# Optimization experiments

Measured on AMD Instinct MI355X. Metric: run time of the kernel, lower is better.

Reference implementation:

```python
import jax, jax.numpy as jnp
import numpy as np

B, S, C, D, H, FF, DEPTH, T, N = 8, 1024, 2, 512, 8, 2048, 6, 64, 16
HD = D // H
EPS = 1e-5


def _ln(x, w, b):
    m = jnp.mean(x, axis=-1, keepdims=True)
    v = jnp.mean(jnp.square(x - m), axis=-1, keepdims=True)
    return (x - m) * jax.lax.rsqrt(v + EPS) * w + b


def setup_inputs() -> dict:
    key = jax.random.key(0)
    ks = jax.random.split(key, 24)
    w = lambda k, shape: (jax.random.normal(k, shape, jnp.float32) * 0.02)
    return {
        "src": jax.random.normal(ks[0], (B, S, D), jnp.float32),
        "ctx_emb": jax.random.normal(ks[1], (B, C, D), jnp.float32),
        "times": jax.random.randint(ks[2], (B, S), 0, T),
        "spaces": jax.random.randint(ks[3], (B, S), 0, N),
        "pad_mask": jnp.zeros((B, S + C), bool),
        "time_emb": w(ks[4], (T, D)),
        "space_emb": w(ks[5], (N, D)),
        "Wqkv": w(ks[6], (DEPTH, 3 * D, D)),
        "bqkv": jnp.zeros((DEPTH, 3 * D), jnp.float32),
        "Wo": w(ks[7], (DEPTH, D, D)),
        "bo": jnp.zeros((DEPTH, D), jnp.float32),
        "ln1_w": jnp.ones((DEPTH, D), jnp.float32),
        "ln1_b": jnp.zeros((DEPTH, D), jnp.float32),
        "W1": w(ks[8], (DEPTH, FF, D)),
        "b1": jnp.zeros((DEPTH, FF), jnp.float32),
        "W2": w(ks[9], (DEPTH, D, FF)),
        "b2": jnp.zeros((DEPTH, D), jnp.float32),
        "ln2_w": jnp.ones((DEPTH, D), jnp.float32),
        "ln2_b": jnp.zeros((DEPTH, D), jnp.float32),
    }


def _forward(src, ctx_emb, times, spaces, pad_mask, time_emb, space_emb,
             Wqkv, bqkv, Wo, bo, ln1_w, ln1_b, W1, b1, W2, b2, ln2_w, ln2_b):
    NEG = -jnp.inf
    # learned time/space positional embeddings, then append context tokens
    x = src + time_emb[times] + space_emb[spaces]          # [B,S,D]
    x = jnp.concatenate([x, ctx_emb], axis=1)              # [B,L,D], L=S+C
    # per-batch additive float mask: causal-in-time over src tokens,
    # ctx tokens attendable by everyone, ctx rows attend only to ctx.
    cond = times[:, :, None] >= times[:, None, :]          # [B,S,S]
    m = jnp.where(cond, 0.0, NEG)
    m = jnp.pad(m, ((0, 0), (0, C), (0, 0)), constant_values=NEG)  # ctx rows
    m = jnp.pad(m, ((0, 0), (0, 0), (0, C)), constant_values=0.0)  # ctx cols
    m = m + jnp.where(pad_mask[:, None, :], NEG, 0.0)      # key padding
    m = m[:, None]                                         # [B,1,L,L]

    scale = 1.0 / np.sqrt(HD)
    Bc, L, _ = x.shape
    for i in range(DEPTH):
        # --- self-attention (post-norm encoder layer) ---
        qkv = x @ Wqkv[i].T + bqkv[i]                      # [B,L,3D]
        q, k, v = jnp.split(qkv, 3, axis=-1)
        split = lambda t: t.reshape(Bc, L, H, HD).transpose(0, 2, 1, 3)
        q, k, v = split(q), split(k), split(v)             # [B,H,L,HD]
        scores = jnp.einsum('bhqd,bhkd->bhqk', q, k) * scale + m
        p = jax.nn.softmax(scores, axis=-1)
        a = jnp.einsum('bhqk,bhkd->bhqd', p, v)
        a = a.transpose(0, 2, 1, 3).reshape(Bc, L, D)
        a = a @ Wo[i].T + bo[i]
        x = _ln(x + a, ln1_w[i], ln1_b[i])
        # --- feed-forward ---
        h = jax.nn.gelu(x @ W1[i].T + b1[i], approximate=False)
        h = h @ W2[i].T + b2[i]
        x = _ln(x + h, ln2_w[i], ln2_b[i])
    return x[:, :S]                                        # drop ctx tokens


def reference(src, ctx_emb, times, spaces, pad_mask, time_emb, space_emb,
              Wqkv, bqkv, Wo, bo, ln1_w, ln1_b, W1, b1, W2, b2, ln2_w, ln2_b):
    return _forward(src, ctx_emb, times, spaces, pad_mask, time_emb, space_emb,
                    Wqkv, bqkv, Wo, bo, ln1_w, ln1_b, W1, b1, W2, b2, ln2_w, ln2_b)
```

## Files before the change

### kernel.cpp

```cpp
#include <hip/hip_runtime.h>
#include <hip/hip_bf16.h>

#define BB 8
#define SS 1024
#define CC 2
#define DD 512
#define NH 8
#define FF2 2048
#define NL 6
#define LL 1026
#define HD 64
#define MROWS 8208
#define MP 8320
#define KVPAD 1152

typedef __attribute__((ext_vector_type(8))) short bf16x8;
typedef __attribute__((ext_vector_type(4))) float f32x4;

typedef __attribute__((address_space(3))) void lds_void;
typedef __attribute__((address_space(1))) void g_void;

__device__ __forceinline__ void gll16(const void* g, void* l) {
  __builtin_amdgcn_global_load_lds((const g_void*)g, (lds_void*)l, 16, 0, 0);
}

__global__ __launch_bounds__(256) void cvt_bf16_k(const float* __restrict__ in,
                                                  __hip_bfloat16* __restrict__ out) {
  int i = (blockIdx.x * 256 + threadIdx.x) * 4;
  float4 v = *(const float4*)&in[i];
  out[i + 0] = __float2bfloat16(v.x);
  out[i + 1] = __float2bfloat16(v.y);
  out[i + 2] = __float2bfloat16(v.z);
  out[i + 3] = __float2bfloat16(v.w);
}

__global__ __launch_bounds__(256) void embed_k(const float* __restrict__ src,
    const float* __restrict__ ctx, const int* __restrict__ times,
    const int* __restrict__ spaces, const float* __restrict__ te,
    const float* __restrict__ se, float* __restrict__ x,
    __hip_bfloat16* __restrict__ xb) {
  int row = blockIdx.x;
  int b = row / LL, l = row % LL;
  int c = threadIdx.x * 2;
  float y0, y1;
  if (l < SS) {
    const float* sp = src + ((size_t)(b * SS + l)) * DD + c;
    int tt = times[b * SS + l], ssp = spaces[b * SS + l];
    y0 = sp[0] + te[tt * DD + c] + se[ssp * DD + c];
    y1 = sp[1] + te[tt * DD + c + 1] + se[ssp * DD + c + 1];
  } else {
    const float* cp = ctx + ((size_t)(b * CC + (l - SS))) * DD + c;
    y0 = cp[0]; y1 = cp[1];
  }
  size_t o = (size_t)row * DD + c;
  x[o] = y0; x[o + 1] = y1;
  xb[o] = __float2bfloat16(y0); xb[o + 1] = __float2bfloat16(y1);
}

template <int EPI>
__global__ __launch_bounds__(256) void gemm_bt(const __hip_bfloat16* __restrict__ A,
    const __hip_bfloat16* __restrict__ W, const float* __restrict__ bias,
    void* __restrict__ outp, int K, int N) {
  __shared__ __hip_bfloat16 As[128 * 64];
  __shared__ __hip_bfloat16 Bs[128 * 64];
  const int tid = threadIdx.x;
  const int lane = tid & 63, wv = tid >> 6;
  const int m0 = blockIdx.x * 128, n0 = blockIdx.y * 128;
  const int wr = wv >> 1, wc = wv & 1;
  const int r0 = lane & 15, kq = lane >> 4;
  f32x4 acc[4][4] = {};
  for (int k0 = 0; k0 < K; k0 += 64) {
    __syncthreads();
#pragma unroll
    for (int c = 0; c < 4; ++c) {
      int chb = c * 256 + wv * 64;
      int ch = chb + lane;
      int row = ch >> 3, cp = ch & 7;
      gll16(A + (size_t)(m0 + row) * K + k0 + cp * 8, (char*)As + chb * 16);
      gll16(W + (size_t)(n0 + row) * K + k0 + cp * 8, (char*)Bs + chb * 16);
    }
    __syncthreads();
#pragma unroll
    for (int kk = 0; kk < 64; kk += 32) {
      bf16x8 af[4], bfr[4];
#pragma unroll
      for (int m = 0; m < 4; ++m)
        af[m] = *(const bf16x8*)&As[(wr * 64 + m * 16 + r0) * 64 + kk + kq * 8];
#pragma unroll
      for (int n = 0; n < 4; ++n)
        bfr[n] = *(const bf16x8*)&Bs[(wc * 64 + n * 16 + r0) * 64 + kk + kq * 8];
#pragma unroll
      for (int m = 0; m < 4; ++m)
#pragma unroll
        for (int n = 0; n < 4; ++n)
          acc[m][n] = __builtin_amdgcn_mfma_f32_16x16x32_bf16(af[m], bfr[n], acc[m][n], 0, 0, 0);
    }
  }
#pragma unroll
  for (int m = 0; m < 4; ++m) {
    int grow_base = m0 + wr * 64 + m * 16 + kq * 4;
#pragma unroll
    for (int n = 0; n < 4; ++n) {
      int gcol = n0 + wc * 64 + n * 16 + r0;
      float bv = bias[gcol];
#pragma unroll
      for (int j = 0; j < 4; ++j) {
        int grow = grow_base + j;
        float v = acc[m][n][j] + bv;
        if (EPI == 2) v = 0.5f * v * (1.f + erff(v * 0.70710678f));
        if (EPI == 0)
          ((float*)outp)[(size_t)grow * N + gcol] = v;
        else
          ((__hip_bfloat16*)outp)[(size_t)grow * N + gcol] = __float2bfloat16(v);
      }
    }
  }
}

__global__ __launch_bounds__(256) void vtrans_k(const __hip_bfloat16* __restrict__ qkv,
                                                __hip_bfloat16* __restrict__ vt) {
  __shared__ __hip_bfloat16 tile[64][72];
  int bh = blockIdx.y;
  int b = bh >> 3, hh = bh & 7;
  int l0 = blockIdx.x * 64;
  int t = threadIdx.x;
  int lr = t >> 2, part = t & 3;
  int l = l0 + lr;
  if (l < LL) {
    const __hip_bfloat16* p = qkv + (size_t)(b * LL + l) * 1536 + 1024 + hh * 64 + part * 16;
    *(uint4*)&tile[lr][part * 16] = *(const uint4*)p;
    *(uint4*)&tile[lr][part * 16 + 8] = *(const uint4*)(p + 8);
  } else {
    uint4 z = make_uint4(0, 0, 0, 0);
    *(uint4*)&tile[lr][part * 16] = z;
    *(uint4*)&tile[lr][part * 16 + 8] = z;
  }
  __syncthreads();
  int d = t >> 2, kp = t & 3;
  __hip_bfloat16 vals[16];
#pragma unroll
  for (int i = 0; i < 16; ++i) vals[i] = tile[kp * 16 + i][d];
  __hip_bfloat16* o = vt + ((size_t)(bh * 64 + d)) * KVPAD + l0 + kp * 16;
  *(uint4*)o = *(uint4*)&vals[0];
  *(uint4*)(o + 8) = *(uint4*)&vals[8];
}

#define TK_CTX (-2000000000)
#define TQ_CTX (-1000000000)
#define TK_INV (2000000000)

__global__ __launch_bounds__(256) void attn_k(const __hip_bfloat16* __restrict__ qkv,
    const __hip_bfloat16* __restrict__ vt, const int* __restrict__ times,
    __hip_bfloat16* __restrict__ aout) {
  __shared__ __hip_bfloat16 Kl[128 * 64];
  __shared__ __hip_bfloat16 Vl[64 * 128];
  __shared__ __hip_bfloat16 Pl[4][16 * 128];
  const int tid = threadIdx.x, lane = tid & 63, wv = tid >> 6;
  const int r0 = lane & 15, kq = lane >> 4;
  int i = blockIdx.x;
  int xcd = i & 7, slot = i >> 3;
  int bhl = slot / 17;
  int qb = slot - bhl * 17;
  int bh = xcd * 8 + bhl;
  int b = bh >> 3, hh = bh & 7;
  char* plbase = (char*)&Pl[wv][0];

  const int qbase = qb * 64 + wv * 16;
  int qr = qbase + r0;
  if (qr > LL - 1) qr = LL - 1;
  const __hip_bfloat16* qp = qkv + (size_t)(b * LL + qr) * 1536 + hh * 64;
  bf16x8 qa0 = *(const bf16x8*)(qp + kq * 8);
  bf16x8 qa1 = *(const bf16x8*)(qp + 32 + kq * 8);
  int tq[4];
#pragma unroll
  for (int j = 0; j < 4; ++j) {
    int r = qbase + kq * 4 + j;
    tq[j] = (r < SS) ? times[b * SS + r] : TQ_CTX;
  }
  float m_run[4] = {-1e30f, -1e30f, -1e30f, -1e30f};
  float l_run[4] = {0.f, 0.f, 0.f, 0.f};
  f32x4 O[4] = {};
  const float scale = 0.125f;

  for (int kc = 0; kc < 9; ++kc) {
    __syncthreads();
#pragma unroll
    for (int c = 0; c < 4; ++c) {
      int chb = c * 256 + wv * 64;
      int ch = chb + lane;
      {
        int trow = ch >> 3, cp = ch & 7;
        int krow = kc * 128 + trow;
        if (krow > LL - 1) krow = LL - 1;
        int scp = cp ^ (trow & 7);
        gll16(qkv + (size_t)(b * LL + krow) * 1536 + 512 + hh * 64 + scp * 8,
              (char*)Kl + chb * 16);
      }
      {
        int d = ch >> 4, kp = ch & 15;
        int skp = kp ^ (d & 7);
        gll16(vt + ((size_t)(bh * 64 + d)) * KVPAD + kc * 128 + skp * 8,
              (char*)Vl + chb * 16);
      }
    }
    __syncthreads();
    f32x4 s[8] = {};
#pragma unroll
    for (int n = 0; n < 8; ++n) {
      int row = n * 16 + r0;
      bf16x8 kb0 = *(const bf16x8*)&Kl[row * 64 + ((kq ^ (row & 7)) * 8)];
      bf16x8 kb1 = *(const bf16x8*)&Kl[row * 64 + (((4 + kq) ^ (row & 7)) * 8)];
      s[n] = __builtin_amdgcn_mfma_f32_16x16x32_bf16(qa0, kb0, s[n], 0, 0, 0);
      s[n] = __builtin_amdgcn_mfma_f32_16x16x32_bf16(qa1, kb1, s[n], 0, 0, 0);
    }
    int tkn[8];
#pragma unroll
    for (int n = 0; n < 8; ++n) {
      int k = kc * 128 + 16 * n + r0;
      tkn[n] = (k < SS) ? times[b * SS + k] : ((k < LL) ? TK_CTX : TK_INV);
    }
    float mch[4] = {-1e30f, -1e30f, -1e30f, -1e30f};
#pragma unroll
    for (int n = 0; n < 8; ++n)
#pragma unroll
      for (int j = 0; j < 4; ++j) {
        float sv = (tq[j] >= tkn[n]) ? s[n][j] * scale : -1e30f;
        s[n][j] = sv;
        mch[j] = fmaxf(mch[j], sv);
      }
#pragma unroll
    for (int j = 0; j < 4; ++j) {
#pragma unroll
      for (int off = 1; off < 16; off <<= 1)
        mch[j] = fmaxf(mch[j], __shfl_xor(mch[j], off, 64));
    }
    float fac[4], psum[4];
#pragma unroll
    for (int j = 0; j < 4; ++j) {
      float mn = fmaxf(m_run[j], mch[j]);
      fac[j] = __expf(m_run[j] - mn);
      m_run[j] = mn;
      psum[j] = 0.f;
    }
#pragma unroll
    for (int n = 0; n < 8; ++n)
#pragma unroll
      for (int j = 0; j < 4; ++j) {
        float p = __expf(s[n][j] - m_run[j]);
        s[n][j] = p;
        psum[j] += p;
      }
#pragma unroll
    for (int j = 0; j < 4; ++j) {
#pragma unroll
      for (int off = 1; off < 16; off <<= 1)
        psum[j] += __shfl_xor(psum[j], off, 64);
      l_run[j] = l_run[j] * fac[j] + psum[j];
    }
#pragma unroll
    for (int n = 0; n < 4; ++n)
#pragma unroll
      for (int j = 0; j < 4; ++j) O[n][j] *= fac[j];
#pragma unroll
    for (int n = 0; n < 8; ++n)
#pragma unroll
      for (int j = 0; j < 4; ++j) {
        int q = kq * 4 + j;
        int byte = ((r0 + 16 * n) * 2) ^ ((q & 7) << 4);
        *(__hip_bfloat16*)(plbase + q * 256 + byte) = __float2bfloat16(s[n][j]);
      }
#pragma unroll
    for (int c = 0; c < 4; ++c) {
      int rbyte = (c * 64 + kq * 16) ^ ((r0 & 7) << 4);
      bf16x8 pa = *(const bf16x8*)(plbase + r0 * 256 + rbyte);
#pragma unroll
      for (int n = 0; n < 4; ++n) {
        int d = n * 16 + r0;
        int chv = (c * 4 + kq) ^ (r0 & 7);
        bf16x8 vb = *(const bf16x8*)&Vl[d * 128 + chv * 8];
        O[n] = __builtin_amdgcn_mfma_f32_16x16x32_bf16(pa, vb, O[n], 0, 0, 0);
      }
    }
  }
#pragma unroll
  for (int j = 0; j < 4; ++j) {
    int orow = qbase + kq * 4 + j;
    if (orow < LL) {
      float inv = 1.f / l_run[j];
#pragma unroll
      for (int n = 0; n < 4; ++n)
        aout[(size_t)(b * LL + orow) * DD + hh * 64 + n * 16 + r0] =
            __float2bfloat16(O[n][j] * inv);
    }
  }
}

__global__ __launch_bounds__(256) void ln_fuse_k(float* __restrict__ x,
    const float* __restrict__ tmp, const float* __restrict__ w,
    const float* __restrict__ bias, __hip_bfloat16* __restrict__ xb) {
  const int row = blockIdx.x;
  const int tid = threadIdx.x;
  size_t o = (size_t)row * DD + tid * 2;
  float2 v = *(const float2*)&x[o];
  float2 t = *(const float2*)&tmp[o];
  float a0 = v.x + t.x, a1 = v.y + t.y;
  float s = a0 + a1, ss = a0 * a0 + a1 * a1;
#pragma unroll
  for (int off = 1; off < 64; off <<= 1) {
    s += __shfl_xor(s, off, 64);
    ss += __shfl_xor(ss, off, 64);
  }
  __shared__ float red[8];
  const int wv = tid >> 6, lane = tid & 63;
  if (lane == 0) { red[wv] = s; red[4 + wv] = ss; }
  __syncthreads();
  s = red[0] + red[1] + red[2] + red[3];
  ss = red[4] + red[5] + red[6] + red[7];
  float mean = s * (1.f / 512.f);
  float var = ss * (1.f / 512.f) - mean * mean;
  if (var < 0.f) var = 0.f;
  float rs = rsqrtf(var + 1e-5f);
  float w0 = w[tid * 2], w1 = w[tid * 2 + 1];
  float b0 = bias[tid * 2], b1 = bias[tid * 2 + 1];
  float y0 = (a0 - mean) * rs * w0 + b0;
  float y1 = (a1 - mean) * rs * w1 + b1;
  x[o] = y0; x[o + 1] = y1;
  xb[o] = __float2bfloat16(y0); xb[o + 1] = __float2bfloat16(y1);
}

__global__ __launch_bounds__(256) void copy_out_k(const float* __restrict__ x,
                                                  float* __restrict__ out) {
  size_t i = ((size_t)blockIdx.x * 256 + threadIdx.x) * 4;
  int b = (int)(i >> 19);
  int rem = (int)(i & 524287);
  float4 v = *(const float4*)&x[(size_t)b * LL * DD + rem];
  *(float4*)&out[i] = v;
}

extern "C" void kernel_launch(void* const* d_in, const int* in_sizes, int n_in,
                              void* d_out, int out_size, void* d_ws, size_t ws_size,
                              hipStream_t stream) {
  (void)in_sizes; (void)n_in; (void)out_size; (void)ws_size;
  const float* src    = (const float*)d_in[0];
  const float* ctx    = (const float*)d_in[1];
  const int*   times  = (const int*)d_in[2];
  const int*   spaces = (const int*)d_in[3];
  const float* te     = (const float*)d_in[5];
  const float* se     = (const float*)d_in[6];
  const float* Wqkv   = (const float*)d_in[7];
  const float* bqkv   = (const float*)d_in[8];
  const float* Wo     = (const float*)d_in[9];
  const float* bo     = (const float*)d_in[10];
  const float* ln1w   = (const float*)d_in[11];
  const float* ln1b   = (const float*)d_in[12];
  const float* W1     = (const float*)d_in[13];
  const float* b1     = (const float*)d_in[14];
  const float* W2     = (const float*)d_in[15];
  const float* b2     = (const float*)d_in[16];
  const float* ln2w   = (const float*)d_in[17];
  const float* ln2b   = (const float*)d_in[18];

  char* ws = (char*)d_ws;
  size_t off = 0;
  auto alloc = [&](size_t bytes) {
    size_t o = off;
    off += (bytes + 255) & ~(size_t)255;
    return o;
  };
  float* x            = (float*)(ws + alloc((size_t)MP * DD * 4));
  __hip_bfloat16* xb  = (__hip_bfloat16*)(ws + alloc((size_t)MP * DD * 2));
  __hip_bfloat16* qkv = (__hip_bfloat16*)(ws + alloc((size_t)MP * 3 * DD * 2));
  __hip_bfloat16* abf = (__hip_bfloat16*)(ws + alloc((size_t)MP * DD * 2));
  __hip_bfloat16* hbf = (__hip_bfloat16*)(ws + alloc((size_t)MP * FF2 * 2));
  float* tmp          = (float*)(ws + alloc((size_t)MP * DD * 4));
  __hip_bfloat16* vt  = (__hip_bfloat16*)(ws + alloc((size_t)BB * NH * HD * KVPAD * 2));
  __hip_bfloat16* wqb = (__hip_bfloat16*)(ws + alloc((size_t)NL * 3 * DD * DD * 2));
  __hip_bfloat16* wob = (__hip_bfloat16*)(ws + alloc((size_t)NL * DD * DD * 2));
  __hip_bfloat16* w1b = (__hip_bfloat16*)(ws + alloc((size_t)NL * FF2 * DD * 2));
  __hip_bfloat16* w2b = (__hip_bfloat16*)(ws + alloc((size_t)NL * DD * FF2 * 2));

  cvt_bf16_k<<<(NL * 3 * DD * DD) / 1024, 256, 0, stream>>>(Wqkv, wqb);
  cvt_bf16_k<<<(NL * DD * DD) / 1024, 256, 0, stream>>>(Wo, wob);
  cvt_bf16_k<<<(NL * FF2 * DD) / 1024, 256, 0, stream>>>(W1, w1b);
  cvt_bf16_k<<<(NL * DD * FF2) / 1024, 256, 0, stream>>>(W2, w2b);

  embed_k<<<MROWS, 256, 0, stream>>>(src, ctx, times, spaces, te, se, x, xb);

  for (int i = 0; i < NL; ++i) {
    gemm_bt<1><<<dim3(MP / 128, 12), 256, 0, stream>>>(
        xb, wqb + (size_t)i * 3 * DD * DD, bqkv + i * 3 * DD, qkv, DD, 3 * DD);
    vtrans_k<<<dim3(17, BB * NH), 256, 0, stream>>>(qkv, vt);
    attn_k<<<1088, 256, 0, stream>>>(qkv, vt, times, abf);
    gemm_bt<0><<<dim3(MP / 128, 4), 256, 0, stream>>>(
        abf, wob + (size_t)i * DD * DD, bo + i * DD, tmp, DD, DD);
    ln_fuse_k<<<MROWS, 256, 0, stream>>>(x, tmp, ln1w + i * DD, ln1b + i * DD, xb);
    gemm_bt<2><<<dim3(MP / 128, 16), 256, 0, stream>>>(
        xb, w1b + (size_t)i * FF2 * DD, b1 + i * FF2, hbf, DD, FF2);
    gemm_bt<0><<<dim3(MP / 128, 4), 256, 0, stream>>>(
        hbf, w2b + (size_t)i * DD * FF2, b2 + i * DD, tmp, FF2, DD);
    ln_fuse_k<<<MROWS, 256, 0, stream>>>(x, tmp, ln2w + i * DD, ln2b + i * DD, xb);
  }

  copy_out_k<<<(BB * SS * DD) / 1024, 256, 0, stream>>>(x, (float*)d_out);
}
```

Measured before the change: 1.563 ms.

## Double-buffer LDS tiles in GEMM to overlap global loads with MFMA

The bf16 GEMM kernel now keeps two LDS buffers for the A and W tiles. It issues the direct-to-LDS load of the next K tile before running the MFMAs on the current one, so memory latency is hidden behind compute. This replaces two barriers per iteration with one explicit vmcnt wait plus a barrier. It doubles LDS use to 64KB per block and adds a launch bound of two blocks per CU, which may limit registers or occupancy.

```diff
diff --git a/kernel.cpp b/kernel.cpp
--- a/kernel.cpp
+++ b/kernel.cpp
@@ -58,44 +58,60 @@
 }
 
 template <int EPI>
-__global__ __launch_bounds__(256) void gemm_bt(const __hip_bfloat16* __restrict__ A,
+__global__ __launch_bounds__(256, 2) void gemm_bt(const __hip_bfloat16* __restrict__ A,
     const __hip_bfloat16* __restrict__ W, const float* __restrict__ bias,
     void* __restrict__ outp, int K, int N) {
-  __shared__ __hip_bfloat16 As[128 * 64];
-  __shared__ __hip_bfloat16 Bs[128 * 64];
+  __shared__ __hip_bfloat16 As[2][128 * 64];
+  __shared__ __hip_bfloat16 Bs[2][128 * 64];
   const int tid = threadIdx.x;
   const int lane = tid & 63, wv = tid >> 6;
   const int m0 = blockIdx.x * 128, n0 = blockIdx.y * 128;
   const int wr = wv >> 1, wc = wv & 1;
   const int r0 = lane & 15, kq = lane >> 4;
   f32x4 acc[4][4] = {};
-  for (int k0 = 0; k0 < K; k0 += 64) {
-    __syncthreads();
+  const int nt = K >> 6;
+
+  auto STAGE = [&](int nb, int t) {
 #pragma unroll
     for (int c = 0; c < 4; ++c) {
       int chb = c * 256 + wv * 64;
       int ch = chb + lane;
       int row = ch >> 3, cp = ch & 7;
-      gll16(A + (size_t)(m0 + row) * K + k0 + cp * 8, (char*)As + chb * 16);
-      gll16(W + (size_t)(n0 + row) * K + k0 + cp * 8, (char*)Bs + chb * 16);
-    }
-    __syncthreads();
+      gll16(A + (size_t)(m0 + row) * K + t * 64 + cp * 8, (char*)&As[nb][0] + chb * 16);
+      gll16(W + (size_t)(n0 + row) * K + t * 64 + cp * 8, (char*)&Bs[nb][0] + chb * 16);
+    }
+  };
+  auto COMPUTE = [&](int nb) {
 #pragma unroll
     for (int kk = 0; kk < 64; kk += 32) {
       bf16x8 af[4], bfr[4];
 #pragma unroll
       for (int m = 0; m < 4; ++m)
-        af[m] = *(const bf16x8*)&As[(wr * 64 + m * 16 + r0) * 64 + kk + kq * 8];
+        af[m] = *(const bf16x8*)&As[nb][(wr * 64 + m * 16 + r0) * 64 + kk + kq * 8];
 #pragma unroll
       for (int n = 0; n < 4; ++n)
-        bfr[n] = *(const bf16x8*)&Bs[(wc * 64 + n * 16 + r0) * 64 + kk + kq * 8];
+        bfr[n] = *(const bf16x8*)&Bs[nb][(wc * 64 + n * 16 + r0) * 64 + kk + kq * 8];
 #pragma unroll
       for (int m = 0; m < 4; ++m)
 #pragma unroll
         for (int n = 0; n < 4; ++n)
           acc[m][n] = __builtin_amdgcn_mfma_f32_16x16x32_bf16(af[m], bfr[n], acc[m][n], 0, 0, 0);
     }
-  }
+  };
+
+  STAGE(0, 0);
+  asm volatile("s_waitcnt vmcnt(0)" ::: "memory");
+  __builtin_amdgcn_s_barrier();
+  int cur = 0;
+  for (int t = 0; t < nt - 1; ++t) {
+    STAGE(cur ^ 1, t + 1);
+    COMPUTE(cur);
+    asm volatile("s_waitcnt vmcnt(0)" ::: "memory");
+    __builtin_amdgcn_s_barrier();
+    cur ^= 1;
+  }
+  COMPUTE(cur);
+
 #pragma unroll
   for (int m = 0; m < 4; ++m) {
     int grow_base = m0 + wr * 64 + m * 16 + kq * 4;
```

After: 1.712 ms. +9.5%, slower.

## Split-K for narrow GEMMs and XCD-aware block remapping

Applied to the files above, without the earlier changes.

The Wo and W2 GEMMs (N=512) now use split-K across blockIdx.y, writing partial fp32 slices that the layernorm kernel sums together with the bias. The goal is more workgroups on the narrow GEMMs, which launched only 260 tiles before. All GEMMs also remap a linear block index so each XCD gets a contiguous run of tiles, for better L2 locality. The cost is extra partial-result memory traffic, and the split factor depends on how much workspace remains.

```diff
diff --git a/kernel.cpp b/kernel.cpp
--- a/kernel.cpp
+++ b/kernel.cpp
@@ -60,16 +60,22 @@
 template <int EPI>
 __global__ __launch_bounds__(256) void gemm_bt(const __hip_bfloat16* __restrict__ A,
     const __hip_bfloat16* __restrict__ W, const float* __restrict__ bias,
-    void* __restrict__ outp, int K, int N) {
+    void* __restrict__ outp, int K, int Ksub, int N) {
   __shared__ __hip_bfloat16 As[128 * 64];
   __shared__ __hip_bfloat16 Bs[128 * 64];
   const int tid = threadIdx.x;
   const int lane = tid & 63, wv = tid >> 6;
-  const int m0 = blockIdx.x * 128, n0 = blockIdx.y * 128;
+  const int ny = N >> 7;
+  const int nwg = gridDim.x;
+  int qq = nwg >> 3, rr = nwg & 7;
+  int xcd = blockIdx.x & 7, loc = blockIdx.x >> 3;
+  int slot = (xcd < rr ? xcd * (qq + 1) : rr * (qq + 1) + (xcd - rr) * qq) + loc;
+  const int m0 = (slot / ny) * 128, n0 = (slot % ny) * 128;
   const int wr = wv >> 1, wc = wv & 1;
   const int r0 = lane & 15, kq = lane >> 4;
+  const int kbeg = blockIdx.y * Ksub, kend = kbeg + Ksub;
   f32x4 acc[4][4] = {};
-  for (int k0 = 0; k0 < K; k0 += 64) {
+  for (int k0 = kbeg; k0 < kend; k0 += 64) {
     __syncthreads();
 #pragma unroll
     for (int c = 0; c < 4; ++c) {
@@ -96,20 +102,21 @@
           acc[m][n] = __builtin_amdgcn_mfma_f32_16x16x32_bf16(af[m], bfr[n], acc[m][n], 0, 0, 0);
     }
   }
+  float* outF = (float*)outp + (size_t)blockIdx.y * MP * N;
 #pragma unroll
   for (int m = 0; m < 4; ++m) {
     int grow_base = m0 + wr * 64 + m * 16 + kq * 4;
 #pragma unroll
     for (int n = 0; n < 4; ++n) {
       int gcol = n0 + wc * 64 + n * 16 + r0;
-      float bv = bias[gcol];
+      float bv = (EPI == 0) ? 0.f : bias[gcol];
 #pragma unroll
       for (int j = 0; j < 4; ++j) {
         int grow = grow_base + j;
         float v = acc[m][n][j] + bv;
         if (EPI == 2) v = 0.5f * v * (1.f + erff(v * 0.70710678f));
         if (EPI == 0)
-          ((float*)outp)[(size_t)grow * N + gcol] = v;
+          outF[(size_t)grow * N + gcol] = v;
         else
           ((__hip_bfloat16*)outp)[(size_t)grow * N + gcol] = __float2bfloat16(v);
       }
@@ -296,14 +303,18 @@
 }
 
 __global__ __launch_bounds__(256) void ln_fuse_k(float* __restrict__ x,
-    const float* __restrict__ tmp, const float* __restrict__ w,
-    const float* __restrict__ bias, __hip_bfloat16* __restrict__ xb) {
+    const float* __restrict__ tmp, int nsplit, const float* __restrict__ gb,
+    const float* __restrict__ w, const float* __restrict__ bias,
+    __hip_bfloat16* __restrict__ xb) {
   const int row = blockIdx.x;
   const int tid = threadIdx.x;
   size_t o = (size_t)row * DD + tid * 2;
   float2 v = *(const float2*)&x[o];
-  float2 t = *(const float2*)&tmp[o];
-  float a0 = v.x + t.x, a1 = v.y + t.y;
+  float a0 = v.x + gb[tid * 2], a1 = v.y + gb[tid * 2 + 1];
+  for (int sp = 0; sp < nsplit; ++sp) {
+    float2 t = *(const float2*)&tmp[(size_t)sp * MP * DD + o];
+    a0 += t.x; a1 += t.y;
+  }
   float s = a0 + a1, ss = a0 * a0 + a1 * a1;
 #pragma unroll
   for (int off = 1; off < 64; off <<= 1) {
@@ -340,7 +351,7 @@
 extern "C" void kernel_launch(void* const* d_in, const int* in_sizes, int n_in,
                               void* d_out, int out_size, void* d_ws, size_t ws_size,
                               hipStream_t stream) {
-  (void)in_sizes; (void)n_in; (void)out_size; (void)ws_size;
+  (void)in_sizes; (void)n_in; (void)out_size;
   const float* src    = (const float*)d_in[0];
   const float* ctx    = (const float*)d_in[1];
   const int*   times  = (const int*)d_in[2];
@@ -372,12 +383,16 @@
   __hip_bfloat16* qkv = (__hip_bfloat16*)(ws + alloc((size_t)MP * 3 * DD * 2));
   __hip_bfloat16* abf = (__hip_bfloat16*)(ws + alloc((size_t)MP * DD * 2));
   __hip_bfloat16* hbf = (__hip_bfloat16*)(ws + alloc((size_t)MP * FF2 * 2));
-  float* tmp          = (float*)(ws + alloc((size_t)MP * DD * 4));
   __hip_bfloat16* vt  = (__hip_bfloat16*)(ws + alloc((size_t)BB * NH * HD * KVPAD * 2));
   __hip_bfloat16* wqb = (__hip_bfloat16*)(ws + alloc((size_t)NL * 3 * DD * DD * 2));
   __hip_bfloat16* wob = (__hip_bfloat16*)(ws + alloc((size_t)NL * DD * DD * 2));
   __hip_bfloat16* w1b = (__hip_bfloat16*)(ws + alloc((size_t)NL * FF2 * DD * 2));
   __hip_bfloat16* w2b = (__hip_bfloat16*)(ws + alloc((size_t)NL * DD * FF2 * 2));
+  const size_t sliceB = (size_t)MP * DD * 4;
+  float* tmp = (float*)(ws + off);
+  size_t remB = (ws_size > off) ? (ws_size - off) : 0;
+  int sW2 = (remB >= 4 * sliceB) ? 4 : 1;
+  int sWo = (remB >= 2 * sliceB) ? 2 : 1;
 
   cvt_bf16_k<<<(NL * 3 * DD * DD) / 1024, 256, 0, stream>>>(Wqkv, wqb);
   cvt_bf16_k<<<(NL * DD * DD) / 1024, 256, 0, stream>>>(Wo, wob);
@@ -387,18 +402,20 @@
   embed_k<<<MROWS, 256, 0, stream>>>(src, ctx, times, spaces, te, se, x, xb);
 
   for (int i = 0; i < NL; ++i) {
-    gemm_bt<1><<<dim3(MP / 128, 12), 256, 0, stream>>>(
-        xb, wqb + (size_t)i * 3 * DD * DD, bqkv + i * 3 * DD, qkv, DD, 3 * DD);
+    gemm_bt<1><<<dim3(65 * 12, 1), 256, 0, stream>>>(
+        xb, wqb + (size_t)i * 3 * DD * DD, bqkv + i * 3 * DD, qkv, DD, DD, 3 * DD);
     vtrans_k<<<dim3(17, BB * NH), 256, 0, stream>>>(qkv, vt);
     attn_k<<<1088, 256, 0, stream>>>(qkv, vt, times, abf);
-    gemm_bt<0><<<dim3(MP / 128, 4), 256, 0, stream>>>(
-        abf, wob + (size_t)i * DD * DD, bo + i * DD, tmp, DD, DD);
-    ln_fuse_k<<<MROWS, 256, 0, stream>>>(x, tmp, ln1w + i * DD, ln1b + i * DD, xb);
-    gemm_bt<2><<<dim3(MP / 128, 16), 256, 0, stream>>>(
-        xb, w1b + (size_t)i * FF2 * DD, b1 + i * FF2, hbf, DD, FF2);
-    gemm_bt<0><<<dim3(MP / 128, 4), 256, 0, stream>>>(
-        hbf, w2b + (size_t)i * DD * FF2, b2 + i * DD, tmp, FF2, DD);
-    ln_fuse_k<<<MROWS, 256, 0, stream>>>(x, tmp, ln2w + i * DD, ln2b + i * DD, xb);
+    gemm_bt<0><<<dim3(65 * 4, sWo), 256, 0, stream>>>(
+        abf, wob + (size_t)i * DD * DD, nullptr, tmp, DD, DD / sWo, DD);
+    ln_fuse_k<<<MROWS, 256, 0, stream>>>(x, tmp, sWo, bo + i * DD,
+                                         ln1w + i * DD, ln1b + i * DD, xb);
+    gemm_bt<2><<<dim3(65 * 16, 1), 256, 0, stream>>>(
+        xb, w1b + (size_t)i * FF2 * DD, b1 + i * FF2, hbf, DD, DD, FF2);
+    gemm_bt<0><<<dim3(65 * 4, sW2), 256, 0, stream>>>(
+        hbf, w2b + (size_t)i * DD * FF2, nullptr, tmp, FF2, FF2 / sW2, DD);
+    ln_fuse_k<<<MROWS, 256, 0, stream>>>(x, tmp, sW2, b2 + i * DD,
+                                         ln2w + i * DD, ln2b + i * DD, xb);
   }
 
   copy_out_k<<<(BB * SS * DD) / 1024, 256, 0, stream>>>(x, (float*)d_out);
```

Measured after the change: 1.587 ms. About the same (+1.5%).

## Remap GEMM blocks XCD-aware, shrink attention key tile, move output bias to LN

Applied to the files above, without the earlier changes.

The GEMM kernel now runs on a 1D grid. Each block's tile index is remapped so that consecutive tiles of the same M rows land on the same XCD, which is meant to improve L2 reuse of A and W. The attention kernel switches from 128-key chunks to 64-key chunks (18 iterations), cutting LDS use and register pressure per block at the cost of more barriers and loop overhead. The fp32-output GEMMs now skip the bias add, and the bias is folded into the layernorm residual kernel instead.

```diff
diff --git a/kernel.cpp b/kernel.cpp
--- a/kernel.cpp
+++ b/kernel.cpp
@@ -65,7 +65,12 @@
   __shared__ __hip_bfloat16 Bs[128 * 64];
   const int tid = threadIdx.x;
   const int lane = tid & 63, wv = tid >> 6;
-  const int m0 = blockIdx.x * 128, n0 = blockIdx.y * 128;
+  const int ny = N >> 7;
+  const int nwg = gridDim.x;
+  int qq = nwg >> 3, rr = nwg & 7;
+  int xcd = blockIdx.x & 7, loc = blockIdx.x >> 3;
+  int slot = (xcd < rr ? xcd * (qq + 1) : rr * (qq + 1) + (xcd - rr) * qq) + loc;
+  const int m0 = (slot / ny) * 128, n0 = (slot % ny) * 128;
   const int wr = wv >> 1, wc = wv & 1;
   const int r0 = lane & 15, kq = lane >> 4;
   f32x4 acc[4][4] = {};
@@ -102,7 +107,7 @@
 #pragma unroll
     for (int n = 0; n < 4; ++n) {
       int gcol = n0 + wc * 64 + n * 16 + r0;
-      float bv = bias[gcol];
+      float bv = (EPI == 0) ? 0.f : bias[gcol];
 #pragma unroll
       for (int j = 0; j < 4; ++j) {
         int grow = grow_base + j;
@@ -152,9 +157,9 @@
 __global__ __launch_bounds__(256) void attn_k(const __hip_bfloat16* __restrict__ qkv,
     const __hip_bfloat16* __restrict__ vt, const int* __restrict__ times,
     __hip_bfloat16* __restrict__ aout) {
-  __shared__ __hip_bfloat16 Kl[128 * 64];
-  __shared__ __hip_bfloat16 Vl[64 * 128];
-  __shared__ __hip_bfloat16 Pl[4][16 * 128];
+  __shared__ __hip_bfloat16 Kl[64 * 64];
+  __shared__ __hip_bfloat16 Vl[64 * 64];
+  __shared__ __hip_bfloat16 Pl[4][16 * 64];
   const int tid = threadIdx.x, lane = tid & 63, wv = tid >> 6;
   const int r0 = lane & 15, kq = lane >> 4;
   int i = blockIdx.x;
@@ -182,46 +187,46 @@
   f32x4 O[4] = {};
   const float scale = 0.125f;
 
-  for (int kc = 0; kc < 9; ++kc) {
+  for (int kc = 0; kc < 18; ++kc) {
     __syncthreads();
 #pragma unroll
-    for (int c = 0; c < 4; ++c) {
+    for (int c = 0; c < 2; ++c) {
       int chb = c * 256 + wv * 64;
       int ch = chb + lane;
       {
         int trow = ch >> 3, cp = ch & 7;
-        int krow = kc * 128 + trow;
+        int krow = kc * 64 + trow;
         if (krow > LL - 1) krow = LL - 1;
         int scp = cp ^ (trow & 7);
         gll16(qkv + (size_t)(b * LL + krow) * 1536 + 512 + hh * 64 + scp * 8,
               (char*)Kl + chb * 16);
       }
       {
-        int d = ch >> 4, kp = ch & 15;
+        int d = ch >> 3, kp = ch & 7;
         int skp = kp ^ (d & 7);
-        gll16(vt + ((size_t)(bh * 64 + d)) * KVPAD + kc * 128 + skp * 8,
+        gll16(vt + ((size_t)(bh * 64 + d)) * KVPAD + kc * 64 + skp * 8,
               (char*)Vl + chb * 16);
       }
     }
     __syncthreads();
-    f32x4 s[8] = {};
-#pragma unroll
-    for (int n = 0; n < 8; ++n) {
+    f32x4 s[4] = {};
+#pragma unroll
+    for (int n = 0; n < 4; ++n) {
       int row = n * 16 + r0;
       bf16x8 kb0 = *(const bf16x8*)&Kl[row * 64 + ((kq ^ (row & 7)) * 8)];
       bf16x8 kb1 = *(const bf16x8*)&Kl[row * 64 + (((4 + kq) ^ (row & 7)) * 8)];
       s[n] = __builtin_amdgcn_mfma_f32_16x16x32_bf16(qa0, kb0, s[n], 0, 0, 0);
       s[n] = __builtin_amdgcn_mfma_f32_16x16x32_bf16(qa1, kb1, s[n], 0, 0, 0);
     }
-    int tkn[8];
-#pragma unroll
-    for (int n = 0; n < 8; ++n) {
-      int k = kc * 128 + 16 * n + r0;
+    int tkn[4];
+#pragma unroll
+    for (int n = 0; n < 4; ++n) {
+      int k = kc * 64 + 16 * n + r0;
       tkn[n] = (k < SS) ? times[b * SS + k] : ((k < LL) ? TK_CTX : TK_INV);
     }
     float mch[4] = {-1e30f, -1e30f, -1e30f, -1e30f};
 #pragma unroll
-    for (int n = 0; n < 8; ++n)
+    for (int n = 0; n < 4; ++n)
 #pragma unroll
       for (int j = 0; j < 4; ++j) {
         float sv = (tq[j] >= tkn[n]) ? s[n][j] * scale : -1e30f;
@@ -243,7 +248,7 @@
       psum[j] = 0.f;
     }
 #pragma unroll
-    for (int n = 0; n < 8; ++n)
+    for (int n = 0; n < 4; ++n)
 #pragma unroll
       for (int j = 0; j < 4; ++j) {
         float p = __expf(s[n][j] - m_run[j]);
@@ -262,22 +267,22 @@
 #pragma unroll
       for (int j = 0; j < 4; ++j) O[n][j] *= fac[j];
 #pragma unroll
-    for (int n = 0; n < 8; ++n)
+    for (int n = 0; n < 4; ++n)
 #pragma unroll
       for (int j = 0; j < 4; ++j) {
         int q = kq * 4 + j;
         int byte = ((r0 + 16 * n) * 2) ^ ((q & 7) << 4);
-        *(__hip_bfloat16*)(plbase + q * 256 + byte) = __float2bfloat16(s[n][j]);
-      }
-#pragma unroll
-    for (int c = 0; c < 4; ++c) {
+        *(__hip_bfloat16*)(plbase + q * 128 + byte) = __float2bfloat16(s[n][j]);
+      }
+#pragma unroll
+    for (int c = 0; c < 2; ++c) {
       int rbyte = (c * 64 + kq * 16) ^ ((r0 & 7) << 4);
-      bf16x8 pa = *(const bf16x8*)(plbase + r0 * 256 + rbyte);
+      bf16x8 pa = *(const bf16x8*)(plbase + r0 * 128 + rbyte);
 #pragma unroll
       for (int n = 0; n < 4; ++n) {
         int d = n * 16 + r0;
         int chv = (c * 4 + kq) ^ (r0 & 7);
-        bf16x8 vb = *(const bf16x8*)&Vl[d * 128 + chv * 8];
+        bf16x8 vb = *(const bf16x8*)&Vl[d * 64 + chv * 8];
         O[n] = __builtin_amdgcn_mfma_f32_16x16x32_bf16(pa, vb, O[n], 0, 0, 0);
       }
     }
@@ -296,14 +301,15 @@
 }
 
 __global__ __launch_bounds__(256) void ln_fuse_k(float* __restrict__ x,
-    const float* __restrict__ tmp, const float* __restrict__ w,
-    const float* __restrict__ bias, __hip_bfloat16* __restrict__ xb) {
+    const float* __restrict__ tmp, const float* __restrict__ gb,
+    const float* __restrict__ w, const float* __restrict__ bias,
+    __hip_bfloat16* __restrict__ xb) {
   const int row = blockIdx.x;
   const int tid = threadIdx.x;
   size_t o = (size_t)row * DD + tid * 2;
   float2 v = *(const float2*)&x[o];
   float2 t = *(const float2*)&tmp[o];
-  float a0 = v.x + t.x, a1 = v.y + t.y;
+  float a0 = v.x + gb[tid * 2] + t.x, a1 = v.y + gb[tid * 2 + 1] + t.y;
   float s = a0 + a1, ss = a0 * a0 + a1 * a1;
 #pragma unroll
   for (int off = 1; off < 64; off <<= 1) {
@@ -387,18 +393,20 @@
   embed_k<<<MROWS, 256, 0, stream>>>(src, ctx, times, spaces, te, se, x, xb);
 
   for (int i = 0; i < NL; ++i) {
-    gemm_bt<1><<<dim3(MP / 128, 12), 256, 0, stream>>>(
+    gemm_bt<1><<<65 * 12, 256, 0, stream>>>(
         xb, wqb + (size_t)i * 3 * DD * DD, bqkv + i * 3 * DD, qkv, DD, 3 * DD);
     vtrans_k<<<dim3(17, BB * NH), 256, 0, stream>>>(qkv, vt);
     attn_k<<<1088, 256, 0, stream>>>(qkv, vt, times, abf);
-    gemm_bt<0><<<dim3(MP / 128, 4), 256, 0, stream>>>(
-        abf, wob + (size_t)i * DD * DD, bo + i * DD, tmp, DD, DD);
-    ln_fuse_k<<<MROWS, 256, 0, stream>>>(x, tmp, ln1w + i * DD, ln1b + i * DD, xb);
-    gemm_bt<2><<<dim3(MP / 128, 16), 256, 0, stream>>>(
+    gemm_bt<0><<<65 * 4, 256, 0, stream>>>(
+        abf, wob + (size_t)i * DD * DD, nullptr, tmp, DD, DD);
+    ln_fuse_k<<<MROWS, 256, 0, stream>>>(x, tmp, bo + i * DD,
+                                         ln1w + i * DD, ln1b + i * DD, xb);
+    gemm_bt<2><<<65 * 16, 256, 0, stream>>>(
         xb, w1b + (size_t)i * FF2 * DD, b1 + i * FF2, hbf, DD, FF2);
-    gemm_bt<0><<<dim3(MP / 128, 4), 256, 0, stream>>>(
-        hbf, w2b + (size_t)i * DD * FF2, b2 + i * DD, tmp, FF2, DD);
-    ln_fuse_k<<<MROWS, 256, 0, stream>>>(x, tmp, ln2w + i * DD, ln2b + i * DD, xb);
+    gemm_bt<0><<<65 * 4, 256, 0, stream>>>(
+        hbf, w2b + (size_t)i * DD * FF2, nullptr, tmp, FF2, DD);
+    ln_fuse_k<<<MROWS, 256, 0, stream>>>(x, tmp, b2 + i * DD,
+                                         ln2w + i * DD, ln2b + i * DD, xb);
   }
 
   copy_out_k<<<(BB * SS * DD) / 1024, 256, 0, stream>>>(x, (float*)d_out);
```

After: 1.615 ms. 3.3% more time.
